# Performance work log

Measured on AMD Instinct MI355X. Metric: run time of the kernel, lower is better.

The kernel has to match this reference:

```python
import jax, jax.numpy as jnp
import numpy as np

N = 100000
E = 1600000
D = 128
EPS = 1e-5


def setup_inputs() -> dict:
    key = jax.random.key(0)
    ks = jax.random.split(key, 6)
    X = jax.random.normal(ks[0], (N, D), dtype=jnp.float32)
    edge_weight = jax.random.uniform(ks[1], (E,), dtype=jnp.float32)
    W = jax.random.normal(ks[2], (2 * D, D), dtype=jnp.float32) * (1.0 / np.sqrt(2 * D))
    b = jax.random.normal(ks[3], (D,), dtype=jnp.float32) * 0.01
    gamma = jnp.ones((D,), dtype=jnp.float32)
    beta = jnp.zeros((D,), dtype=jnp.float32)
    edge_src = jax.random.randint(ks[4], (E,), 0, N, dtype=jnp.int32)
    edge_dst = jax.random.randint(ks[5], (E,), 0, N, dtype=jnp.int32)
    return {"X": X, "edge_weight": edge_weight, "W": W, "b": b,
            "gamma": gamma, "beta": beta,
            "edge_src": edge_src, "edge_dst": edge_dst}


def reference(X, edge_weight, W, b, gamma, beta, edge_src, edge_dst):
    # Pre-LayerNorm over feature dim
    mu = jnp.mean(X, axis=-1, keepdims=True)
    var = jnp.mean(jnp.square(X - mu), axis=-1, keepdims=True)
    H = (X - mu) * jax.lax.rsqrt(var + EPS) * gamma + beta
    # dropout is identity in eval mode
    # sparse neighbor aggregation: neigh[i] = sum_{e: dst[e]=i} w[e] * H[src[e]]
    msgs = edge_weight[:, None] * H[edge_src]          # [E, D]
    neigh = jax.ops.segment_sum(msgs, edge_dst, num_segments=X.shape[0])  # [N, D]
    cat = jnp.concatenate([H, neigh], axis=1)          # [N, 2D]
    out = cat @ W + b                                  # [N, D]
    out = jax.nn.relu(out)
    return out + X                                     # residual (in_dim == out_dim)
```

## Files before the change

### kernel.cpp

```cpp
#include <hip/hip_runtime.h>
#include <hip/hip_bf16.h>

#define N_NODES 100000
#define D 128
#define E_EDGES 1600000

#define BSHIFT 6
#define BROWS 64
#define NBUCK 1563
#define NBUCKP 1600
#define CAP 2304
#define SRTCAP 1536
#define NBLK_S 256
#define SBLK 1024
#define EPB (E_EDGES / NBLK_S)
#define LN_BLOCKS ((N_NODES + 15) / 16)

typedef __attribute__((ext_vector_type(8))) short bf16x8;
typedef __attribute__((ext_vector_type(8))) unsigned short ushort8;
typedef __attribute__((ext_vector_type(4))) float f32x4;

__device__ __forceinline__ float bf2f(unsigned short u) {
    unsigned int x = ((unsigned int)u) << 16;
    return __builtin_bit_cast(float, x);
}
__device__ __forceinline__ unsigned short f2bf(float f) {
    unsigned int x = __builtin_bit_cast(unsigned int, f);
    unsigned int lsb = (x >> 16) & 1u;
    x += 0x7fffu + lsb;
    return (unsigned short)(x >> 16);
}

__global__ __launch_bounds__(256) void wt_kernel(
    const float* __restrict__ W, unsigned short* __restrict__ Wt)
{
    int i = blockIdx.x * 1024 + threadIdx.x * 4;
    #pragma unroll
    for (int j = 0; j < 4; ++j) {
        int idx = i + j;
        int k = idx >> 7, col = idx & 127;
        Wt[col * 256 + k] = f2bf(W[idx]);
    }
}

__global__ __launch_bounds__(1024) void fused_ln_scatter(
    const float* __restrict__ X,
    const float* __restrict__ gamma,
    const float* __restrict__ beta,
    unsigned short* __restrict__ H,
    const int* __restrict__ esrc, const int* __restrict__ edst,
    const float* __restrict__ ew,
    unsigned int* __restrict__ gcur,
    uint2* __restrict__ bins)
{
    __shared__ uint2 ent[EPB];
    __shared__ unsigned int hh[NBUCKP];
    __shared__ unsigned int lofs[NBUCKP];
    __shared__ unsigned int cur[NBUCKP];
    __shared__ unsigned int ctot[32];

    if (blockIdx.x < NBLK_S) {
        const int t    = threadIdx.x;
        const int wv   = t >> 6;
        const int lane = t & 63;
        const int base = blockIdx.x * EPB;

        for (int i = t; i < NBUCKP; i += SBLK) hh[i] = 0;
        __syncthreads();
        for (int k = t; k < EPB; k += SBLK)
            atomicAdd(&hh[edst[base + k] >> BSHIFT], 1u);
        __syncthreads();

        for (int c = wv; c < 25; c += 16) {
            unsigned int v = hh[c * 64 + lane];
            unsigned int inc = v;
            #pragma unroll
            for (int off = 1; off < 64; off <<= 1) {
                unsigned int u = __shfl_up(inc, off);
                if (lane >= off) inc += u;
            }
            lofs[c * 64 + lane] = inc - v;
            if (lane == 63) ctot[c] = inc;
        }
        __syncthreads();
        if (wv == 0) {
            unsigned int v = (lane < 25) ? ctot[lane] : 0u;
            unsigned int inc = v;
            #pragma unroll
            for (int off = 1; off < 32; off <<= 1) {
                unsigned int u = __shfl_up(inc, off);
                if (lane >= off) inc += u;
            }
            if (lane < 25) ctot[lane] = inc - v;
        }
        __syncthreads();
        for (int i = t; i < NBUCKP; i += SBLK) lofs[i] += ctot[i >> 6];
        __syncthreads();

        for (int i = t; i < NBUCK; i += SBLK) {
            unsigned int c = hh[i];
            if (c) hh[i] = atomicAdd(&gcur[i], (c + 7u) & ~7u);
            cur[i] = lofs[i];
        }
        __syncthreads();

        for (int k = t; k < EPB; k += SBLK) {
            int e = base + k;
            int d = edst[e];
            int bkt = d >> BSHIFT;
            unsigned int p = atomicAdd(&cur[bkt], 1u);
            ent[p] = make_uint2((unsigned int)esrc[e] |
                                ((unsigned int)(d & (BROWS - 1)) << 17),
                                __builtin_bit_cast(unsigned int, ew[e]));
        }
        __syncthreads();

        for (int b = wv; b < NBUCK; b += 16) {
            unsigned int l0 = lofs[b];
            unsigned int c  = cur[b] - l0;
            if (!c) continue;
            unsigned int cround = (c + 7u) & ~7u;
            unsigned int gb = hh[b];
            for (unsigned int j = lane; j < cround; j += 64) {
                uint2 v = (j < c) ? ent[l0 + j] : make_uint2(0u, 0u);
                unsigned int slot = gb + j;
                if (slot < CAP)
                    bins[(size_t)b * CAP + slot] = v;
            }
        }
    } else {
        int wid  = (blockIdx.x - NBLK_S) * (SBLK / 64) + (threadIdx.x >> 6);
        int lane = threadIdx.x & 63;
        if (wid >= N_NODES) return;

        const float2 x2 = *reinterpret_cast<const float2*>(X + (size_t)wid * D + 2 * lane);
        float x0 = x2.x, x1 = x2.y;
        float s  = x0 + x1;
        float sq = x0 * x0 + x1 * x1;
        #pragma unroll
        for (int m = 1; m < 64; m <<= 1) {
            s  += __shfl_xor(s,  m);
            sq += __shfl_xor(sq, m);
        }
        float mu   = s * (1.0f / 128.0f);
        float var  = sq * (1.0f / 128.0f) - mu * mu;
        float rstd = rsqrtf(var + 1e-5f);

        const float2 g2 = *reinterpret_cast<const float2*>(gamma + 2 * lane);
        const float2 b2 = *reinterpret_cast<const float2*>(beta  + 2 * lane);

        ushort2 h2;
        h2.x = f2bf((x0 - mu) * rstd * g2.x + b2.x);
        h2.y = f2bf((x1 - mu) * rstd * g2.y + b2.y);
        *reinterpret_cast<ushort2*>(H + (size_t)wid * D + 2 * lane) = h2;
    }
}

__global__ __launch_bounds__(256) void sort_aggregate(
    const unsigned short* __restrict__ H,
    const uint2* __restrict__ bins,
    const unsigned int* __restrict__ gcur,
    unsigned short* __restrict__ nb)
{
    __shared__ uint2 srt[SRTCAP];
    __shared__ unsigned int cnt[BROWS];
    __shared__ unsigned int cur[BROWS];
    __shared__ unsigned int starts[BROWS + 1];

    const int b = blockIdx.x;
    const int t = threadIdx.x;
    const unsigned int gbase = (unsigned int)b * CAP;
    const int nE = (int)min(gcur[b], (unsigned int)CAP);

    if (t < BROWS) cnt[t] = 0;
    __syncthreads();

    for (int k = t; k < nE; k += 256) {
        uint2 r = bins[gbase + k];
        if (r.y) atomicAdd(&cnt[r.x >> 17], 1u);
    }
    __syncthreads();

    if (t < BROWS) {
        unsigned int v = cnt[t], inc = v;
        #pragma unroll
        for (int off = 1; off < BROWS; off <<= 1) {
            unsigned int u = __shfl_up(inc, off);
            if (t >= off) inc += u;
        }
        unsigned int start = inc - v;
        starts[t] = start;
        cur[t] = start;
        if (t == BROWS - 1) starts[BROWS] = inc;
    }
    __syncthreads();

    for (int k = t; k < nE; k += 256) {
        uint2 r = bins[gbase + k];
        if (r.y) {
            unsigned int p = atomicAdd(&cur[r.x >> 17], 1u);
            if (p < SRTCAP) srt[p] = make_uint2(r.x & 0x1FFFFu, r.y);
        }
    }
    __syncthreads();

    const int wv      = t >> 6;
    const int lane    = t & 63;
    const int quarter = lane >> 4;
    const int l15     = lane & 15;

    for (int j = 0; j < 16; ++j) {
        const int nl   = wv * 16 + j;
        const int node = b * BROWS + nl;
        if (node >= N_NODES) break;
        const int s = (int)starts[nl];
        const int n = (int)starts[nl + 1] - s;

        float a0 = 0.f, a1 = 0.f, a2 = 0.f, a3 = 0.f;
        float a4 = 0.f, a5 = 0.f, a6 = 0.f, a7 = 0.f;

        int k = 0;
        for (; k + 8 <= n; k += 8) {
            uint2 r0 = srt[s + k + quarter];
            uint2 r1 = srt[s + k + 4 + quarter];
            ushort8 h0 = *reinterpret_cast<const ushort8*>(H + (size_t)r0.x * D + 8 * l15);
            ushort8 h1 = *reinterpret_cast<const ushort8*>(H + (size_t)r1.x * D + 8 * l15);
            float w0 = __builtin_bit_cast(float, r0.y);
            float w1 = __builtin_bit_cast(float, r1.y);
            a0 += w0 * bf2f(h0[0]) + w1 * bf2f(h1[0]);
            a1 += w0 * bf2f(h0[1]) + w1 * bf2f(h1[1]);
            a2 += w0 * bf2f(h0[2]) + w1 * bf2f(h1[2]);
            a3 += w0 * bf2f(h0[3]) + w1 * bf2f(h1[3]);
            a4 += w0 * bf2f(h0[4]) + w1 * bf2f(h1[4]);
            a5 += w0 * bf2f(h0[5]) + w1 * bf2f(h1[5]);
            a6 += w0 * bf2f(h0[6]) + w1 * bf2f(h1[6]);
            a7 += w0 * bf2f(h0[7]) + w1 * bf2f(h1[7]);
        }
        if (k + 4 <= n) {
            uint2 r0 = srt[s + k + quarter];
            ushort8 h0 = *reinterpret_cast<const ushort8*>(H + (size_t)r0.x * D + 8 * l15);
            float w0 = __builtin_bit_cast(float, r0.y);
            a0 += w0 * bf2f(h0[0]); a1 += w0 * bf2f(h0[1]);
            a2 += w0 * bf2f(h0[2]); a3 += w0 * bf2f(h0[3]);
            a4 += w0 * bf2f(h0[4]); a5 += w0 * bf2f(h0[5]);
            a6 += w0 * bf2f(h0[6]); a7 += w0 * bf2f(h0[7]);
            k += 4;
        }
        if (k < n) {
            bool valid = (k + quarter) < n;
            uint2 r0 = srt[valid ? (s + k + quarter) : s];
            ushort8 h0 = *reinterpret_cast<const ushort8*>(H + (size_t)r0.x * D + 8 * l15);
            float w0 = valid ? __builtin_bit_cast(float, r0.y) : 0.f;
            a0 += w0 * bf2f(h0[0]); a1 += w0 * bf2f(h0[1]);
            a2 += w0 * bf2f(h0[2]); a3 += w0 * bf2f(h0[3]);
            a4 += w0 * bf2f(h0[4]); a5 += w0 * bf2f(h0[5]);
            a6 += w0 * bf2f(h0[6]); a7 += w0 * bf2f(h0[7]);
        }

        a0 += __shfl_xor(a0, 16); a0 += __shfl_xor(a0, 32);
        a1 += __shfl_xor(a1, 16); a1 += __shfl_xor(a1, 32);
        a2 += __shfl_xor(a2, 16); a2 += __shfl_xor(a2, 32);
        a3 += __shfl_xor(a3, 16); a3 += __shfl_xor(a3, 32);
        a4 += __shfl_xor(a4, 16); a4 += __shfl_xor(a4, 32);
        a5 += __shfl_xor(a5, 16); a5 += __shfl_xor(a5, 32);
        a6 += __shfl_xor(a6, 16); a6 += __shfl_xor(a6, 32);
        a7 += __shfl_xor(a7, 16); a7 += __shfl_xor(a7, 32);

        if (quarter == 0) {
            ushort8 ov;
            ov[0] = f2bf(a0); ov[1] = f2bf(a1); ov[2] = f2bf(a2); ov[3] = f2bf(a3);
            ov[4] = f2bf(a4); ov[5] = f2bf(a5); ov[6] = f2bf(a6); ov[7] = f2bf(a7);
            *reinterpret_cast<ushort8*>(nb + (size_t)node * D + 8 * l15) = ov;
        }
    }
}

#define ROWS_PER_BLOCK 128
#define STRIPS 8

__global__ __launch_bounds__(256) void gemm_kernel(
    const unsigned short* __restrict__ H,
    const unsigned short* __restrict__ nb,
    const unsigned short* __restrict__ Wt,
    const float* __restrict__ bias,
    const float* __restrict__ X,
    float* __restrict__ out)
{
    __shared__ unsigned short lds[16][256];

    const int tid  = threadIdx.x;
    const int w    = tid >> 6;
    const int lane = tid & 63;
    const int l15  = lane & 15;
    const int l4   = lane >> 4;

    bf16x8 bfrag[2][8];
    #pragma unroll
    for (int t = 0; t < 2; ++t) {
        const int col = 32 * w + 16 * t + l15;
        #pragma unroll
        for (int s = 0; s < 8; ++s)
            bfrag[t][s] = *reinterpret_cast<const bf16x8*>(
                Wt + (size_t)col * 256 + 32 * s + 8 * l4);
    }
    const float bias0 = bias[32 * w + l15];
    const float bias1 = bias[32 * w + 16 + l15];

    const int row0_blk = blockIdx.x * ROWS_PER_BLOCK;

    for (int strip = 0; strip < STRIPS; ++strip) {
        const int r0 = row0_blk + strip * 16;
        __syncthreads();

        {
            const int row  = tid >> 4;
            const int c8   = tid & 15;
            const int grow = r0 + row;
            char* ldsrow = (char*)&lds[row][0];
            const int key = (row & 7) << 4;

            uint4 hv = make_uint4(0u, 0u, 0u, 0u);
            uint4 nv = make_uint4(0u, 0u, 0u, 0u);
            if (grow < N_NODES) {
                hv = *reinterpret_cast<const uint4*>(H  + (size_t)grow * D + 8 * c8);
                nv = *reinterpret_cast<const uint4*>(nb + (size_t)grow * D + 8 * c8);
            }
            *reinterpret_cast<uint4*>(ldsrow + ((16 * c8) ^ key)) = hv;
            *reinterpret_cast<uint4*>(ldsrow + ((256 + 16 * c8) ^ key)) = nv;
        }
        __syncthreads();

        f32x4 acc0 = {0.f, 0.f, 0.f, 0.f};
        f32x4 acc1 = {0.f, 0.f, 0.f, 0.f};
        const char* ldsa = (const char*)&lds[l15][0];
        const int   akey = (l15 & 7) << 4;
        #pragma unroll
        for (int s = 0; s < 8; ++s) {
            bf16x8 afrag = *reinterpret_cast<const bf16x8*>(
                ldsa + ((64 * s + 16 * l4) ^ akey));
            acc0 = __builtin_amdgcn_mfma_f32_16x16x32_bf16(afrag, bfrag[0][s], acc0, 0, 0, 0);
            acc1 = __builtin_amdgcn_mfma_f32_16x16x32_bf16(afrag, bfrag[1][s], acc1, 0, 0, 0);
        }

        #pragma unroll
        for (int r = 0; r < 4; ++r) {
            const int grow = r0 + 4 * l4 + r;
            if (grow < N_NODES) {
                const size_t base = (size_t)grow * D;
                const int c0 = 32 * w + l15;
                float v0 = acc0[r] + bias0;
                v0 = v0 > 0.f ? v0 : 0.f;
                out[base + c0] = v0 + X[base + c0];
                const int c1 = c0 + 16;
                float v1 = acc1[r] + bias1;
                v1 = v1 > 0.f ? v1 : 0.f;
                out[base + c1] = v1 + X[base + c1];
            }
        }
    }
}

extern "C" void kernel_launch(void* const* d_in, const int* in_sizes, int n_in,
                              void* d_out, int out_size, void* d_ws, size_t ws_size,
                              hipStream_t stream)
{
    const float* X     = (const float*)d_in[0];
    const float* ew    = (const float*)d_in[1];
    const float* W     = (const float*)d_in[2];
    const float* b     = (const float*)d_in[3];
    const float* gamma = (const float*)d_in[4];
    const float* beta  = (const float*)d_in[5];
    const int* esrc = (const int*)d_in[6];
    const int* edst = (const int*)d_in[7];
    float* out = (float*)d_out;

    unsigned short* H  = (unsigned short*)d_ws;
    unsigned short* nb = H + (size_t)N_NODES * D;
    uint2* bins = (uint2*)(nb + (size_t)N_NODES * D);
    unsigned int* gcur = (unsigned int*)(bins + (size_t)NBUCK * CAP);
    unsigned short* Wt = (unsigned short*)(gcur + NBUCK + 1);

    hipMemsetAsync(gcur, 0, NBUCK * sizeof(unsigned int), stream);
    wt_kernel<<<32, 256, 0, stream>>>(W, Wt);
    fused_ln_scatter<<<NBLK_S + LN_BLOCKS, SBLK, 0, stream>>>(
        X, gamma, beta, H, esrc, edst, ew, gcur, bins);
    sort_aggregate<<<NBUCK, 256, 0, stream>>>(H, bins, gcur, nb);
    gemm_kernel<<<(N_NODES + ROWS_PER_BLOCK - 1) / ROWS_PER_BLOCK, 256, 0, stream>>>(
        H, nb, Wt, b, X, out);
}
```

Before: 155.2 us.

## Replace global bucket atomics with per-block run table for bucket gather

The scatter blocks no longer reserve space in global per-bucket bins with atomics. Each block now writes its locally sorted edges contiguously and records a per-bucket (offset, count) run table. The aggregate kernel has each of its 256 threads read one source block's run for the bucket, so the global atomics, the memset and the padding are all removed. The cost is serial per-thread loops over short, uncoalesced runs, and the count is clamped at 255, which would drop edges if a run were ever larger.

```diff
diff --git a/kernel.cpp b/kernel.cpp
--- a/kernel.cpp
+++ b/kernel.cpp
@@ -9,8 +9,7 @@
 #define BROWS 64
 #define NBUCK 1563
 #define NBUCKP 1600
-#define CAP 2304
-#define SRTCAP 1536
+#define CAP 1536
 #define NBLK_S 256
 #define SBLK 1024
 #define EPB (E_EDGES / NBLK_S)
@@ -50,7 +49,7 @@
     unsigned short* __restrict__ H,
     const int* __restrict__ esrc, const int* __restrict__ edst,
     const float* __restrict__ ew,
-    unsigned int* __restrict__ gcur,
+    unsigned int* __restrict__ runs,
     uint2* __restrict__ bins)
 {
     __shared__ uint2 ent[EPB];
@@ -94,40 +93,31 @@
             if (lane < 25) ctot[lane] = inc - v;
         }
         __syncthreads();
-        for (int i = t; i < NBUCKP; i += SBLK) lofs[i] += ctot[i >> 6];
-        __syncthreads();
-
-        for (int i = t; i < NBUCK; i += SBLK) {
+        for (int i = t; i < NBUCKP; i += SBLK) {
+            unsigned int l = lofs[i] + ctot[i >> 6];
+            lofs[i] = l;
+            cur[i]  = l;
+        }
+        __syncthreads();
+
+        for (int i = t; i < NBUCKP; i += SBLK) {
             unsigned int c = hh[i];
-            if (c) hh[i] = atomicAdd(&gcur[i], (c + 7u) & ~7u);
-            cur[i] = lofs[i];
-        }
-        __syncthreads();
+            runs[(size_t)blockIdx.x * NBUCKP + i] =
+                (lofs[i] << 8) | (c > 255u ? 255u : c);
+        }
 
         for (int k = t; k < EPB; k += SBLK) {
             int e = base + k;
             int d = edst[e];
-            int bkt = d >> BSHIFT;
-            unsigned int p = atomicAdd(&cur[bkt], 1u);
+            unsigned int p = atomicAdd(&cur[d >> BSHIFT], 1u);
             ent[p] = make_uint2((unsigned int)esrc[e] |
                                 ((unsigned int)(d & (BROWS - 1)) << 17),
                                 __builtin_bit_cast(unsigned int, ew[e]));
         }
         __syncthreads();
 
-        for (int b = wv; b < NBUCK; b += 16) {
-            unsigned int l0 = lofs[b];
-            unsigned int c  = cur[b] - l0;
-            if (!c) continue;
-            unsigned int cround = (c + 7u) & ~7u;
-            unsigned int gb = hh[b];
-            for (unsigned int j = lane; j < cround; j += 64) {
-                uint2 v = (j < c) ? ent[l0 + j] : make_uint2(0u, 0u);
-                unsigned int slot = gb + j;
-                if (slot < CAP)
-                    bins[(size_t)b * CAP + slot] = v;
-            }
-        }
+        for (int k = t; k < EPB; k += SBLK)
+            bins[(size_t)blockIdx.x * EPB + k] = ent[k];
     } else {
         int wid  = (blockIdx.x - NBLK_S) * (SBLK / 64) + (threadIdx.x >> 6);
         int lane = threadIdx.x & 63;
@@ -159,26 +149,27 @@
 __global__ __launch_bounds__(256) void sort_aggregate(
     const unsigned short* __restrict__ H,
     const uint2* __restrict__ bins,
-    const unsigned int* __restrict__ gcur,
+    const unsigned int* __restrict__ runs,
     unsigned short* __restrict__ nb)
 {
-    __shared__ uint2 srt[SRTCAP];
+    __shared__ uint2 srt[CAP];
     __shared__ unsigned int cnt[BROWS];
     __shared__ unsigned int cur[BROWS];
     __shared__ unsigned int starts[BROWS + 1];
 
     const int b = blockIdx.x;
     const int t = threadIdx.x;
-    const unsigned int gbase = (unsigned int)b * CAP;
-    const int nE = (int)min(gcur[b], (unsigned int)CAP);
 
     if (t < BROWS) cnt[t] = 0;
     __syncthreads();
 
-    for (int k = t; k < nE; k += 256) {
-        uint2 r = bins[gbase + k];
-        if (r.y) atomicAdd(&cnt[r.x >> 17], 1u);
-    }
+    const unsigned int r  = runs[(size_t)t * NBUCKP + b];
+    const unsigned int st = r >> 8;
+    const unsigned int c  = r & 255u;
+    const uint2* src = bins + (size_t)t * EPB + st;
+
+    for (unsigned int i = 0; i < c; ++i)
+        atomicAdd(&cnt[src[i].x >> 17], 1u);
     __syncthreads();
 
     if (t < BROWS) {
@@ -195,12 +186,10 @@
     }
     __syncthreads();
 
-    for (int k = t; k < nE; k += 256) {
-        uint2 r = bins[gbase + k];
-        if (r.y) {
-            unsigned int p = atomicAdd(&cur[r.x >> 17], 1u);
-            if (p < SRTCAP) srt[p] = make_uint2(r.x & 0x1FFFFu, r.y);
-        }
+    for (unsigned int i = 0; i < c; ++i) {
+        uint2 e = src[i];
+        unsigned int p = atomicAdd(&cur[e.x >> 17], 1u);
+        if (p < CAP) srt[p] = make_uint2(e.x & 0x1FFFFu, e.y);
     }
     __syncthreads();
 
@@ -377,14 +366,13 @@
     unsigned short* H  = (unsigned short*)d_ws;
     unsigned short* nb = H + (size_t)N_NODES * D;
     uint2* bins = (uint2*)(nb + (size_t)N_NODES * D);
-    unsigned int* gcur = (unsigned int*)(bins + (size_t)NBUCK * CAP);
-    unsigned short* Wt = (unsigned short*)(gcur + NBUCK + 1);
-
-    hipMemsetAsync(gcur, 0, NBUCK * sizeof(unsigned int), stream);
+    unsigned int* runs = (unsigned int*)(bins + (size_t)NBLK_S * EPB);
+    unsigned short* Wt = (unsigned short*)(runs + (size_t)NBLK_S * NBUCKP);
+
     wt_kernel<<<32, 256, 0, stream>>>(W, Wt);
     fused_ln_scatter<<<NBLK_S + LN_BLOCKS, SBLK, 0, stream>>>(
-        X, gamma, beta, H, esrc, edst, ew, gcur, bins);
-    sort_aggregate<<<NBUCK, 256, 0, stream>>>(H, bins, gcur, nb);
+        X, gamma, beta, H, esrc, edst, ew, runs, bins);
+    sort_aggregate<<<NBUCK, 256, 0, stream>>>(H, bins, runs, nb);
     gemm_kernel<<<(N_NODES + ROWS_PER_BLOCK - 1) / ROWS_PER_BLOCK, 256, 0, stream>>>(
         H, nb, Wt, b, X, out);
 }
```

Measured after the change: 154.5 us. No clear change (-0.5%).
